# Performance work log

Measured on AMD Instinct MI355X. Metric: run time of the kernel, lower is better.

## Reference

```python
import jax, jax.numpy as jnp
import numpy as np

B, T, C, H = 4, 1024, 512, 8
HD = C // H
N_NODE, F_DIM, TOTAL_DIM = 64, 8, 16
SCALE = 1.0 / np.sqrt(HD)


def _build_mask():
    # causal tril with every (total_dim-1 mod total_dim)-th COLUMN zeroed
    m = np.tril(np.ones((T, T), dtype=np.float32))
    m[:, TOTAL_DIM - 1::TOTAL_DIM] = 0.0
    return jnp.asarray(m)

MASK = _build_mask()  # (T, T), 1 = keep, 0 = mask


def setup_inputs() -> dict:
    key = jax.random.key(0)
    ks = jax.random.split(key, 12)
    s = 0.02
    return {
        "x": jax.random.normal(ks[0], (B, T, C), dtype=jnp.float32),
        "attn_bias": jax.random.normal(ks[1], (H, N_NODE, N_NODE), dtype=jnp.float32) * 0.1,
        "Wq": jax.random.normal(ks[2], (C, C), dtype=jnp.float32) * s,
        "bq": jax.random.normal(ks[3], (C,), dtype=jnp.float32) * s,
        "Wk": jax.random.normal(ks[4], (C, C), dtype=jnp.float32) * s,
        "bk": jax.random.normal(ks[5], (C,), dtype=jnp.float32) * s,
        "Wv": jax.random.normal(ks[6], (C, C), dtype=jnp.float32) * s,
        "bv": jax.random.normal(ks[7], (C,), dtype=jnp.float32) * s,
        "Wp": jax.random.normal(ks[8], (C, C), dtype=jnp.float32) * s,
        "bp": jax.random.normal(ks[9], (C,), dtype=jnp.float32) * s,
    }


def reference(x, attn_bias, Wq, bq, Wk, bk, Wv, bv, Wp, bp):
    Bx, Tx, Cx = x.shape

    def heads(W, b):  # (B,T,C) -> (B,H,T,HD); torch Linear is x @ W.T + b
        return (x @ W.T + b).reshape(Bx, Tx, H, HD).transpose(0, 2, 1, 3)

    q, k, v = heads(Wq, bq), heads(Wk, bk), heads(Wv, bv)

    # repeat_interleave + repeat expansion == kron(attn_bias, ones(f_dim, f_dim))
    d = N_NODE * F_DIM
    bias = jnp.repeat(jnp.repeat(attn_bias, F_DIM, axis=1), F_DIM, axis=2)  # (H, d, d)
    padded_bias = jnp.zeros((H, Tx, Tx), dtype=x.dtype).at[:, :d, :d].set(bias)

    att = jnp.einsum('bhqd,bhkd->bhqk', q, k) * SCALE + padded_bias[None]
    neg = jnp.asarray(-jnp.inf, dtype=att.dtype)
    att = jnp.where(MASK[None, None, :Tx, :Tx] == 0, neg, att)
    att = jax.nn.softmax(att, axis=-1)

    y = jnp.einsum('bhqk,bhkd->bhqd', att, v)
    y = y.transpose(0, 2, 1, 3).reshape(Bx, Tx, Cx)
    return y @ Wp.T + bp
```

## Files before the change

### kernel.cpp

```cpp
#include <hip/hip_runtime.h>

#define T_SEQ 1024
#define C_DIM 512
#define H_HEADS 8
#define HDIM 64
#define B_BATCH 4
#define M_ROWS (B_BATCH * T_SEQ)
#define NSPLIT_TOT 40

typedef __attribute__((ext_vector_type(8))) short short8;
typedef __attribute__((ext_vector_type(4))) float f32x4;

__device__ __forceinline__ unsigned short f2bf(float f) {
    unsigned u = __builtin_bit_cast(unsigned, f);
    u += 0x7FFFu + ((u >> 16) & 1u);
    return (unsigned short)(u >> 16);
}

__device__ __forceinline__ void gload_lds16(const unsigned short* g, unsigned short* l) {
    __builtin_amdgcn_global_load_lds(
        (const __attribute__((address_space(1))) unsigned int*)(const void*)g,
        (__attribute__((address_space(3))) unsigned int*)(void*)l, 16, 0, 0);
}

__device__ __constant__ unsigned char BX_OF[NSPLIT_TOT] =
    {0,1,2,3,4,4,5,5,6,6,7,7,8,8,8,9,9,9,10,10,10,11,11,11,
     12,12,12,12,13,13,13,13,14,14,14,14,15,15,15,15};
__device__ __constant__ unsigned char SP_OF[NSPLIT_TOT] =
    {0,0,0,0,0,1,0,1,0,1,0,1,0,1,2,0,1,2,0,1,2,0,1,2,
     0,1,2,3,0,1,2,3,0,1,2,3,0,1,2,3};
__device__ __constant__ unsigned char CUM_OF[16] =
    {0,1,2,3,4,6,8,10,12,15,18,21,24,28,32,36};

__global__ __launch_bounds__(256) void cast_all(
    const float* __restrict__ x,
    const float* __restrict__ wq, const float* __restrict__ wk,
    const float* __restrict__ wv, const float* __restrict__ wp,
    unsigned short* __restrict__ xb,
    unsigned short* __restrict__ wqb, unsigned short* __restrict__ wkb,
    unsigned short* __restrict__ wvb, unsigned short* __restrict__ wpb)
{
    const long NX = (long)M_ROWS * C_DIM;
    const long NW = (long)C_DIM * C_DIM;
    long i4 = (long)blockIdx.x * blockDim.x + threadIdx.x;
    long base = i4 * 4;
    const float* src; unsigned short* dst; long off;
    if (base < NX) { src = x; dst = xb; off = base; }
    else {
        long r = base - NX;
        int w = (int)(r >> 18);
        off = r & (NW - 1);
        switch (w) {
            case 0:  src = wq; dst = wqb; break;
            case 1:  src = wk; dst = wkb; break;
            case 2:  src = wv; dst = wvb; break;
            default: src = wp; dst = wpb; break;
        }
    }
    float4 v = *(const float4*)(src + off);
    ushort4 o;
    o.x = f2bf(v.x); o.y = f2bf(v.y); o.z = f2bf(v.z); o.w = f2bf(v.w);
    *(ushort4*)(dst + off) = o;
}

__device__ __forceinline__ void gemm_body(
    const unsigned short* __restrict__ A,
    const unsigned short* __restrict__ W,
    const float* __restrict__ bias,
    unsigned short* __restrict__ Obf,
    float* __restrict__ Of,
    int mode)
{
    __shared__ __align__(16) unsigned short Atile[128 * 64];
    __shared__ __align__(16) unsigned short Btile[128 * 64];

    const int tid  = threadIdx.x;
    const int w    = tid >> 6;
    const int lane = tid & 63;
    const int quad = lane >> 4;
    const int l16  = lane & 15;
    const int m0   = blockIdx.x * 128;
    const int n0   = blockIdx.y * 128;
    const int wr   = 64 * (w >> 1);
    const int wc   = 64 * (w & 1);

    f32x4 acc[4][4] = {};

    const int lr = lane >> 3;
    const int lc = lane & 7;

    for (int k0 = 0; k0 < 512; k0 += 64) {
        __syncthreads();
        for (int i = 0; i < 4; ++i) {
            int r0 = 32 * w + 8 * i;
            int r  = r0 + lr;
            int c  = lc ^ (r & 7);
            gload_lds16(&A[(long)(m0 + r) * 512 + k0 + c * 8], &Atile[r0 * 64]);
            gload_lds16(&W[(long)(n0 + r) * 512 + k0 + c * 8], &Btile[r0 * 64]);
        }
        __syncthreads();

        for (int st = 0; st < 2; ++st) {
            const int pc = ((4 * st + quad) ^ (l16 & 7)) * 8;
            short8 af[4], bf[4];
            for (int i = 0; i < 4; ++i)
                af[i] = *(const short8*)&Atile[(wr + 16 * i + l16) * 64 + pc];
            for (int j = 0; j < 4; ++j)
                bf[j] = *(const short8*)&Btile[(wc + 16 * j + l16) * 64 + pc];
            for (int i = 0; i < 4; ++i)
                for (int j = 0; j < 4; ++j)
                    acc[i][j] = (mode == 1)
                        ? __builtin_amdgcn_mfma_f32_16x16x32_bf16(bf[j], af[i], acc[i][j], 0, 0, 0)
                        : __builtin_amdgcn_mfma_f32_16x16x32_bf16(af[i], bf[j], acc[i][j], 0, 0, 0);
        }
    }

    if (mode == 1) {
        for (int j = 0; j < 4; ++j) {
            for (int reg = 0; reg < 4; ++reg) {
                int n = n0 + wc + 16 * j + 4 * quad + reg;
                int h = n >> 6, hd = n & 63;
                float bv = bias[n];
                for (int i = 0; i < 4; ++i) {
                    int t = m0 + wr + 16 * i + l16;
                    int b = t >> 10, tl = t & 1023;
                    Obf[(((long)(b * H_HEADS + h)) * HDIM + hd) * T_SEQ + tl] =
                        f2bf(acc[i][j][reg] + bv);
                }
            }
        }
    } else {
        for (int j = 0; j < 4; ++j) {
            int col = n0 + wc + 16 * j + l16;
            float bv = bias[col];
            for (int i = 0; i < 4; ++i) {
                for (int reg = 0; reg < 4; ++reg) {
                    int row = m0 + wr + 16 * i + 4 * quad + reg;
                    float v = acc[i][j][reg] + bv;
                    if (mode == 2) {
                        Of[(long)row * 512 + col] = v;
                    } else {
                        int b = row >> 10, t = row & 1023;
                        int h = col >> 6,  hd = col & 63;
                        Obf[(((long)(b * H_HEADS + h)) * T_SEQ + t) * HDIM + hd] = f2bf(v);
                    }
                }
            }
        }
    }
}

__global__ __launch_bounds__(256) void gemm_qkv(
    const unsigned short* __restrict__ A,
    const unsigned short* __restrict__ Wq, const unsigned short* __restrict__ Wk,
    const unsigned short* __restrict__ Wv,
    const float* __restrict__ bq, const float* __restrict__ bk, const float* __restrict__ bv,
    unsigned short* __restrict__ Q, unsigned short* __restrict__ K,
    unsigned short* __restrict__ V)
{
    const unsigned short* W; const float* b; unsigned short* O; int mode;
    if (blockIdx.z == 0)      { W = Wq; b = bq; O = Q; mode = 0; }
    else if (blockIdx.z == 1) { W = Wk; b = bk; O = K; mode = 0; }
    else                      { W = Wv; b = bv; O = V; mode = 1; }
    gemm_body(A, W, b, O, nullptr, mode);
}

__global__ __launch_bounds__(256) void gemm_out_k(
    const unsigned short* __restrict__ A, const unsigned short* __restrict__ W,
    const float* __restrict__ bias, float* __restrict__ O)
{
    gemm_body(A, W, bias, nullptr, O, 2);
}

__global__ __launch_bounds__(256) void attn_split(
    const unsigned short* __restrict__ Q, const unsigned short* __restrict__ K,
    const unsigned short* __restrict__ Vt, const float* __restrict__ attn_bias,
    float* __restrict__ Opart, float* __restrict__ lpart)
{
    __shared__ __align__(16) unsigned short Kl[64 * 72];
    __shared__ __align__(16) unsigned short Vl[64 * 72];
    __shared__ __align__(16) unsigned short Pl[4][16 * 72];
    __shared__ float biasl[8][64];

    const int tid  = threadIdx.x;
    const int w    = tid >> 6;
    const int lane = tid & 63;
    const int quad = lane >> 4;
    const int l16  = lane & 15;
    const int sidx = blockIdx.x;
    const int bh   = blockIdx.y;
    const int h    = bh & 7;
    const int bx   = BX_OF[sidx];
    const int sp   = SP_OF[sidx];
    const int q0   = bx * 64;
    const int kt0  = sp * 4;
    const int kt1  = min(kt0 + 4, bx + 1);
    const bool use_bias = (q0 < 512) && (sp < 2);

    if (use_bias) {
        for (int i = tid; i < 512; i += 256) {
            int nq = (q0 >> 3) + (i >> 6);
            biasl[i >> 6][i & 63] = attn_bias[h * 4096 + nq * 64 + (i & 63)];
        }
    }

    const unsigned short* Qbh = Q  + (long)bh * T_SEQ * HDIM;
    const unsigned short* Kbh = K  + (long)bh * T_SEQ * HDIM;
    const unsigned short* Vbh = Vt + (long)bh * HDIM * T_SEQ;

    short8 qf[2];
    {
        int qr = q0 + 16 * w + l16;
        qf[0] = *(const short8*)&Qbh[(long)qr * HDIM + 8 * quad];
        qf[1] = *(const short8*)&Qbh[(long)qr * HDIM + 32 + 8 * quad];
    }

    f32x4 oacc[4] = {};
    float lrow[4] = {0.f, 0.f, 0.f, 0.f};

    for (int kt = kt0; kt < kt1; ++kt) {
        const int k0 = kt * 64;
        __syncthreads();
        for (int it = 0; it < 2; ++it) {
            int ch = tid + 256 * it;
            int r = ch >> 3, c8 = ch & 7;
            *(short8*)&Kl[r * 72 + c8 * 8] =
                *(const short8*)&Kbh[(long)(k0 + r) * HDIM + c8 * 8];
            *(short8*)&Vl[r * 72 + c8 * 8] =
                *(const short8*)&Vbh[(long)r * T_SEQ + k0 + c8 * 8];
        }
        __syncthreads();

        f32x4 s[4] = {};
        for (int st = 0; st < 2; ++st) {
            for (int ct = 0; ct < 4; ++ct) {
                short8 bf = *(const short8*)&Kl[(16 * ct + l16) * 72 + 32 * st + 8 * quad];
                s[ct] = __builtin_amdgcn_mfma_f32_16x16x32_bf16(qf[st], bf, s[ct], 0, 0, 0);
            }
        }

        const int qrb = q0 + 16 * w + 4 * quad;
        const bool diag = (kt == bx);
        const bool colkeep = (l16 != 15);
        float rsum[4] = {0.f, 0.f, 0.f, 0.f};
        for (int ct = 0; ct < 4; ++ct) {
            int kcol = k0 + 16 * ct + l16;
            for (int reg = 0; reg < 4; ++reg) {
                float v = s[ct][reg] * 0.125f;
                if (use_bias)
                    v += biasl[((qrb + reg) >> 3) & 7][kcol >> 3];
                bool keep = colkeep && (!diag || (kcol <= qrb + reg));
                float p = keep ? __expf(v) : 0.f;
                rsum[reg] += p;
                Pl[w][(4 * quad + reg) * 72 + 16 * ct + l16] = f2bf(p);
            }
        }
        for (int off = 1; off < 16; off <<= 1)
            for (int reg = 0; reg < 4; ++reg)
                rsum[reg] += __shfl_xor(rsum[reg], off);
        for (int reg = 0; reg < 4; ++reg)
            lrow[reg] += rsum[reg];

        for (int st = 0; st < 2; ++st) {
            short8 af = *(const short8*)&Pl[w][l16 * 72 + 32 * st + 8 * quad];
            for (int ct = 0; ct < 4; ++ct) {
                short8 bf = *(const short8*)&Vl[(16 * ct + l16) * 72 + 32 * st + 8 * quad];
                oacc[ct] = __builtin_amdgcn_mfma_f32_16x16x32_bf16(af, bf, oacc[ct], 0, 0, 0);
            }
        }
    }

    const long p = (long)bh * NSPLIT_TOT + sidx;
    float* Op = Opart + p * 4096;
    for (int ct = 0; ct < 4; ++ct)
        for (int reg = 0; reg < 4; ++reg)
            Op[(16 * w + 4 * quad + reg) * 64 + 16 * ct + l16] = oacc[ct][reg];
    if (l16 == 0) {
        for (int reg = 0; reg < 4; ++reg) {
            int qr = 16 * w + 4 * quad + reg;
            lpart[p * 64 + qr] = lrow[reg];
        }
    }
}

__global__ __launch_bounds__(256) void attn_combine(
    const float* __restrict__ Opart, const float* __restrict__ lpart,
    unsigned short* __restrict__ Y)
{
    const int bx = blockIdx.x, bh = blockIdx.y;
    const int b = bh >> 3, h = bh & 7;
    const int ns = (bx >> 2) + 1;
    const long p0 = (long)bh * NSPLIT_TOT + CUM_OF[bx];
    const int tid = threadIdx.x;
    const int qr = tid >> 2;
    const int hs = (tid & 3) * 16;

    float L = 0.f;
    for (int s = 0; s < ns; ++s) L += lpart[(p0 + s) * 64 + qr];

    float acc[16] = {};
    for (int s = 0; s < ns; ++s) {
        const float4* op = (const float4*)(Opart + (p0 + s) * 4096 + qr * 64 + hs);
        for (int j4 = 0; j4 < 4; ++j4) {
            float4 v = op[j4];
            acc[4 * j4 + 0] += v.x; acc[4 * j4 + 1] += v.y;
            acc[4 * j4 + 2] += v.z; acc[4 * j4 + 3] += v.w;
        }
    }
    float inv = 1.f / L;
    int q = bx * 64 + qr;
    unsigned short* y = Y + ((long)b * T_SEQ + q) * C_DIM + h * HDIM + hs;
    for (int j4 = 0; j4 < 4; ++j4) {
        ushort4 o;
        o.x = f2bf(acc[4 * j4 + 0] * inv); o.y = f2bf(acc[4 * j4 + 1] * inv);
        o.z = f2bf(acc[4 * j4 + 2] * inv); o.w = f2bf(acc[4 * j4 + 3] * inv);
        *(ushort4*)(y + 4 * j4) = o;
    }
}

extern "C" void kernel_launch(void* const* d_in, const int* in_sizes, int n_in,
                              void* d_out, int out_size, void* d_ws, size_t ws_size,
                              hipStream_t stream)
{
    const float* x         = (const float*)d_in[0];
    const float* attn_bias = (const float*)d_in[1];
    const float* Wq = (const float*)d_in[2]; const float* bq = (const float*)d_in[3];
    const float* Wk = (const float*)d_in[4]; const float* bk = (const float*)d_in[5];
    const float* Wv = (const float*)d_in[6]; const float* bv = (const float*)d_in[7];
    const float* Wp = (const float*)d_in[8]; const float* bp = (const float*)d_in[9];
    float* out = (float*)d_out;

    const long NX = (long)M_ROWS * C_DIM;
    const long NW = (long)C_DIM * C_DIM;

    unsigned short* xb  = (unsigned short*)d_ws;
    unsigned short* wqb = xb  + NX;
    unsigned short* wkb = wqb + NW;
    unsigned short* wvb = wkb + NW;
    unsigned short* wpb = wvb + NW;
    unsigned short* Qb  = wpb + NW;
    unsigned short* Kb  = Qb  + NX;
    unsigned short* Vtb = Kb  + NX;
    unsigned short* Yb  = Vtb + NX;
    float* Opart = (float*)(Yb + NX);
    float* lpart = Opart + (long)32 * NSPLIT_TOT * 4096;

    long n4 = (NX + 4 * NW) / 4;
    cast_all<<<dim3((unsigned)(n4 / 256)), 256, 0, stream>>>(
        x, Wq, Wk, Wv, Wp, xb, wqb, wkb, wvb, wpb);

    gemm_qkv<<<dim3(M_ROWS / 128, C_DIM / 128, 3), 256, 0, stream>>>(
        xb, wqb, wkb, wvb, bq, bk, bv, Qb, Kb, Vtb);

    attn_split<<<dim3(NSPLIT_TOT, B_BATCH * H_HEADS), 256, 0, stream>>>(
        Qb, Kb, Vtb, attn_bias, Opart, lpart);

    attn_combine<<<dim3(T_SEQ / 64, B_BATCH * H_HEADS), 256, 0, stream>>>(
        Opart, lpart, Yb);

    gemm_out_k<<<dim3(M_ROWS / 128, C_DIM / 128), 256, 0, stream>>>(
        Yb, wpb, bp, out);
}
```

Measured before the change: 137.4 us.

## Replace split-K attention and combine pass with single fused causal attention kernel

Drops the 40-way split of key tiles and the separate combine kernel. Each block now walks all causal key tiles for one 64-row query block and writes normalized bf16 output directly. Blocks are ordered longest-first (reversed bx) to soften the load imbalance. The bias lookup is hoisted per column tile and the row-sum shuffle reduction is deferred to the end. This removes the fp32 partial-output traffic and one kernel launch, but leaves only 512 blocks with unequal work (1 to 16 tiles), so the longest blocks may set the runtime.

```diff
diff --git a/kernel.cpp b/kernel.cpp
--- a/kernel.cpp
+++ b/kernel.cpp
@@ -6,7 +6,6 @@
 #define HDIM 64
 #define B_BATCH 4
 #define M_ROWS (B_BATCH * T_SEQ)
-#define NSPLIT_TOT 40
 
 typedef __attribute__((ext_vector_type(8))) short short8;
 typedef __attribute__((ext_vector_type(4))) float f32x4;
@@ -22,15 +21,6 @@
         (const __attribute__((address_space(1))) unsigned int*)(const void*)g,
         (__attribute__((address_space(3))) unsigned int*)(void*)l, 16, 0, 0);
 }
-
-__device__ __constant__ unsigned char BX_OF[NSPLIT_TOT] =
-    {0,1,2,3,4,4,5,5,6,6,7,7,8,8,8,9,9,9,10,10,10,11,11,11,
-     12,12,12,12,13,13,13,13,14,14,14,14,15,15,15,15};
-__device__ __constant__ unsigned char SP_OF[NSPLIT_TOT] =
-    {0,0,0,0,0,1,0,1,0,1,0,1,0,1,2,0,1,2,0,1,2,0,1,2,
-     0,1,2,3,0,1,2,3,0,1,2,3,0,1,2,3};
-__device__ __constant__ unsigned char CUM_OF[16] =
-    {0,1,2,3,4,6,8,10,12,15,18,21,24,28,32,36};
 
 __global__ __launch_bounds__(256) void cast_all(
     const float* __restrict__ x,
@@ -172,10 +162,10 @@
     gemm_body(A, W, bias, nullptr, O, 2);
 }
 
-__global__ __launch_bounds__(256) void attn_split(
+__global__ __launch_bounds__(256) void attn_fused(
     const unsigned short* __restrict__ Q, const unsigned short* __restrict__ K,
     const unsigned short* __restrict__ Vt, const float* __restrict__ attn_bias,
-    float* __restrict__ Opart, float* __restrict__ lpart)
+    unsigned short* __restrict__ Y)
 {
     __shared__ __align__(16) unsigned short Kl[64 * 72];
     __shared__ __align__(16) unsigned short Vl[64 * 72];
@@ -187,15 +177,12 @@
     const int lane = tid & 63;
     const int quad = lane >> 4;
     const int l16  = lane & 15;
-    const int sidx = blockIdx.x;
+    const int bx   = 15 - blockIdx.x;
     const int bh   = blockIdx.y;
     const int h    = bh & 7;
-    const int bx   = BX_OF[sidx];
-    const int sp   = SP_OF[sidx];
     const int q0   = bx * 64;
-    const int kt0  = sp * 4;
-    const int kt1  = min(kt0 + 4, bx + 1);
-    const bool use_bias = (q0 < 512) && (sp < 2);
+    const bool use_bias = (q0 < 512);
+    const int brow = 2 * w + (quad >> 1);
 
     if (use_bias) {
         for (int i = tid; i < 512; i += 256) {
@@ -217,8 +204,9 @@
 
     f32x4 oacc[4] = {};
     float lrow[4] = {0.f, 0.f, 0.f, 0.f};
-
-    for (int kt = kt0; kt < kt1; ++kt) {
+    const int qrb = q0 + 16 * w + 4 * quad;
+
+    for (int kt = 0; kt <= bx; ++kt) {
         const int k0 = kt * 64;
         __syncthreads();
         for (int it = 0; it < 2; ++it) {
@@ -239,27 +227,20 @@
             }
         }
 
-        const int qrb = q0 + 16 * w + 4 * quad;
         const bool diag = (kt == bx);
+        const bool addb = use_bias && (kt < 8);
         const bool colkeep = (l16 != 15);
-        float rsum[4] = {0.f, 0.f, 0.f, 0.f};
         for (int ct = 0; ct < 4; ++ct) {
             int kcol = k0 + 16 * ct + l16;
+            float bval = addb ? biasl[brow][(k0 >> 3) + 2 * ct + (l16 >> 3)] : 0.f;
             for (int reg = 0; reg < 4; ++reg) {
-                float v = s[ct][reg] * 0.125f;
-                if (use_bias)
-                    v += biasl[((qrb + reg) >> 3) & 7][kcol >> 3];
+                float v = s[ct][reg] * 0.125f + bval;
                 bool keep = colkeep && (!diag || (kcol <= qrb + reg));
                 float p = keep ? __expf(v) : 0.f;
-                rsum[reg] += p;
+                lrow[reg] += p;
                 Pl[w][(4 * quad + reg) * 72 + 16 * ct + l16] = f2bf(p);
             }
         }
-        for (int off = 1; off < 16; off <<= 1)
-            for (int reg = 0; reg < 4; ++reg)
-                rsum[reg] += __shfl_xor(rsum[reg], off);
-        for (int reg = 0; reg < 4; ++reg)
-            lrow[reg] += rsum[reg];
 
         for (int st = 0; st < 2; ++st) {
             short8 af = *(const short8*)&Pl[w][l16 * 72 + 32 * st + 8 * quad];
@@ -270,51 +251,17 @@
         }
     }
 
-    const long p = (long)bh * NSPLIT_TOT + sidx;
-    float* Op = Opart + p * 4096;
-    for (int ct = 0; ct < 4; ++ct)
+    for (int off = 1; off < 16; off <<= 1)
         for (int reg = 0; reg < 4; ++reg)
-            Op[(16 * w + 4 * quad + reg) * 64 + 16 * ct + l16] = oacc[ct][reg];
-    if (l16 == 0) {
-        for (int reg = 0; reg < 4; ++reg) {
-            int qr = 16 * w + 4 * quad + reg;
-            lpart[p * 64 + qr] = lrow[reg];
-        }
-    }
-}
-
-__global__ __launch_bounds__(256) void attn_combine(
-    const float* __restrict__ Opart, const float* __restrict__ lpart,
-    unsigned short* __restrict__ Y)
-{
-    const int bx = blockIdx.x, bh = blockIdx.y;
-    const int b = bh >> 3, h = bh & 7;
-    const int ns = (bx >> 2) + 1;
-    const long p0 = (long)bh * NSPLIT_TOT + CUM_OF[bx];
-    const int tid = threadIdx.x;
-    const int qr = tid >> 2;
-    const int hs = (tid & 3) * 16;
-
-    float L = 0.f;
-    for (int s = 0; s < ns; ++s) L += lpart[(p0 + s) * 64 + qr];
-
-    float acc[16] = {};
-    for (int s = 0; s < ns; ++s) {
-        const float4* op = (const float4*)(Opart + (p0 + s) * 4096 + qr * 64 + hs);
-        for (int j4 = 0; j4 < 4; ++j4) {
-            float4 v = op[j4];
-            acc[4 * j4 + 0] += v.x; acc[4 * j4 + 1] += v.y;
-            acc[4 * j4 + 2] += v.z; acc[4 * j4 + 3] += v.w;
-        }
-    }
-    float inv = 1.f / L;
-    int q = bx * 64 + qr;
-    unsigned short* y = Y + ((long)b * T_SEQ + q) * C_DIM + h * HDIM + hs;
-    for (int j4 = 0; j4 < 4; ++j4) {
-        ushort4 o;
-        o.x = f2bf(acc[4 * j4 + 0] * inv); o.y = f2bf(acc[4 * j4 + 1] * inv);
-        o.z = f2bf(acc[4 * j4 + 2] * inv); o.w = f2bf(acc[4 * j4 + 3] * inv);
-        *(ushort4*)(y + 4 * j4) = o;
+            lrow[reg] += __shfl_xor(lrow[reg], off);
+
+    const int b = bh >> 3;
+    for (int reg = 0; reg < 4; ++reg) {
+        int qrow = qrb + reg;
+        float inv = 1.f / lrow[reg];
+        unsigned short* y = Y + ((long)b * T_SEQ + qrow) * C_DIM + h * HDIM;
+        for (int ct = 0; ct < 4; ++ct)
+            y[16 * ct + l16] = f2bf(oacc[ct][reg] * inv);
     }
 }
 
@@ -342,8 +289,6 @@
     unsigned short* Kb  = Qb  + NX;
     unsigned short* Vtb = Kb  + NX;
     unsigned short* Yb  = Vtb + NX;
-    float* Opart = (float*)(Yb + NX);
-    float* lpart = Opart + (long)32 * NSPLIT_TOT * 4096;
 
     long n4 = (NX + 4 * NW) / 4;
     cast_all<<<dim3((unsigned)(n4 / 256)), 256, 0, stream>>>(
@@ -352,11 +297,8 @@
     gemm_qkv<<<dim3(M_ROWS / 128, C_DIM / 128, 3), 256, 0, stream>>>(
         xb, wqb, wkb, wvb, bq, bk, bv, Qb, Kb, Vtb);
 
-    attn_split<<<dim3(NSPLIT_TOT, B_BATCH * H_HEADS), 256, 0, stream>>>(
-        Qb, Kb, Vtb, attn_bias, Opart, lpart);
-
-    attn_combine<<<dim3(T_SEQ / 64, B_BATCH * H_HEADS), 256, 0, stream>>>(
-        Opart, lpart, Yb);
+    attn_fused<<<dim3(T_SEQ / 64, B_BATCH * H_HEADS), 256, 0, stream>>>(
+        Qb, Kb, Vtb, attn_bias, Yb);
 
     gemm_out_k<<<dim3(M_ROWS / 128, C_DIM / 128), 256, 0, stream>>>(
         Yb, wpb, bp, out);
```

Measured after the change: 148.9 us. 8.4% more time.
